# Kernel optimization log

Hardware: AMD Instinct MI355X
Metric: run time of the kernel (lower is better)

The kernel has to match this reference:

```python
import jax, jax.numpy as jnp
import numpy as np

B, N, D, R = 4, 50000, 64, 500
E_PER = 62500
E = B * E_PER


def _build_edges():
    rng = np.random.default_rng(0)
    idx = np.repeat(np.arange(B), E_PER)
    vi = rng.integers(0, N, E)
    vj = rng.integers(0, N, E)
    order = np.lexsort((vj, vi, idx))
    idx, vi, vj = idx[order], vi[order], vj[order]
    rel = rng.integers(0, R, E)
    key_vi = idx.astype(np.int64) * N + vi
    _, idx_vi = np.unique(key_vi, return_inverse=True)  # sorted -> nondecreasing segment ids
    key_vj = idx.astype(np.int64) * N + vj
    _, idx_vj = np.unique(key_vj, return_inverse=True)
    all_keys = np.concatenate([key_vi, key_vj])
    uniq_all, inv = np.unique(all_keys, return_inverse=True)
    e2vi, e2vj = inv[:E], inv[E:]
    sel = np.stack([idx, vi, vj, rel, idx_vi, idx_vj, e2vi, e2vj], axis=1).astype(np.int32)
    return sel, int(idx_vi.max() + 1), int(idx_vj.max() + 1), int(len(uniq_all))


def setup_inputs() -> dict:
    sel, n_vi_seg, n_vj_seg, n_visited = _build_edges()
    key = jax.random.key(0)
    ks = jax.random.split(key, 9)
    na = jax.random.uniform(ks[0], (B, N), jnp.float32) + 1e-6
    na = na / jnp.sum(na, axis=1, keepdims=True)
    return {
        'node_attention': na,
        'selected_edges': jnp.asarray(sel),
        'edges_y': jax.random.uniform(ks[1], (E,), jnp.float32, 0.1, 1.0),
        'hidden_con': jax.random.normal(ks[2], (n_visited, D), jnp.float32) * 0.1,
        'hidden_uncon': jax.random.normal(ks[3], (1, N, D), jnp.float32) * 0.1,
        'rel_emb': jax.random.normal(ks[4], (R, D), jnp.float32) * 0.1,
        'ws': jax.random.normal(ks[5], (8, D), jnp.float32) * (1.0 / np.sqrt(8.0)),
        'b': jax.random.normal(ks[6], (D,), jnp.float32) * 0.01,
        'out_w': jax.random.normal(ks[7], (D,), jnp.float32) * 0.3,
        'out_b': jax.random.normal(ks[8], (D,), jnp.float32) * 0.01,
        'n_vi_seg': n_vi_seg,
        'n_vj_seg': n_vj_seg,
    }


def reference(node_attention, selected_edges, edges_y, hidden_con, hidden_uncon,
              rel_emb, ws, b, out_w, out_b, n_vi_seg, n_vj_seg):
    idx, vi, vj = selected_edges[:, 0], selected_edges[:, 1], selected_edges[:, 2]
    rel, idx_vi, idx_vj = selected_edges[:, 3], selected_edges[:, 4], selected_edges[:, 5]
    e2vi, e2vj = selected_edges[:, 6], selected_edges[:, 7]

    # Node2Edge gathers
    hc_vi, hc_vj = hidden_con[e2vi], hidden_con[e2vj]        # [E, D]
    hu = hidden_uncon[0]                                     # hidden_uncon has batch 1
    hu_vi, hu_vj = hu[vi], hu[vj]                            # [E, D]
    re = rel_emb[rel]                                        # [E, D]

    # F layer: interact = [[0,3],[0,2,3],[0,4],[0,2,4],[1,3],[1,2,3],[1,4],[1,2,4]]
    terms = (hc_vi * hc_vj, hc_vi * re * hc_vj, hc_vi * hu_vj, hc_vi * re * hu_vj,
             hu_vi * hc_vj, hu_vi * re * hc_vj, hu_vi * hu_vj, hu_vi * re * hu_vj)
    f = b
    for k in range(8):
        f = f + ws[k] * terms[k]
    f = jax.nn.relu(f) * out_w + out_b                       # [E, D]
    logits = jnp.sum(f, axis=1)                              # [E]

    # NeighborSoftmax at='vi' (segment softmax)
    seg_max = jax.ops.segment_max(logits, idx_vi, num_segments=n_vi_seg)
    e = jnp.exp(logits - seg_max[idx_vi])
    es = jax.ops.segment_sum(e, idx_vi, num_segments=n_vi_seg)
    transition = e / es[idx_vi]

    # attention flow
    na_e = node_attention[idx, vi]
    ta = na_e * transition * edges_y

    # Aggregate at='vj', sum, then scatter into (B, n_nodes)
    aggr = jax.ops.segment_sum(ta, idx_vj, num_segments=n_vj_seg)
    seg_idx = jax.ops.segment_max(idx, idx_vj, num_segments=n_vj_seg)
    seg_vj = jax.ops.segment_max(vj, idx_vj, num_segments=n_vj_seg)
    Bn, Nn = node_attention.shape
    new_att = jnp.zeros((Bn, Nn), node_attention.dtype).at[seg_idx, seg_vj].add(aggr)
    return new_att / jnp.sum(new_att, axis=1, keepdims=True)
```

## Files before the change

### kernel.cpp

```cpp
#include <hip/hip_runtime.h>
#include <math.h>

#define D 64

__global__ __launch_bounds__(256) void k_logits(
    const int* __restrict__ sel, const float* __restrict__ hc,
    const float* __restrict__ hu, const float* __restrict__ re,
    const float* __restrict__ wsm, const float* __restrict__ bias,
    const float* __restrict__ out_w, const float* __restrict__ out_b,
    float* __restrict__ logits, int* __restrict__ seg_start,
    float* __restrict__ out, float* __restrict__ row_sum,
    int E, int BN, int Bn)
{
    const int tid = blockIdx.x * 256 + threadIdx.x;
    const int nthreads = gridDim.x * 256;

    for (int i = tid; i < BN; i += nthreads) out[i] = 0.f;
    if (tid < Bn) row_sum[tid] = 0.f;

    const int lane = threadIdx.x & 63;
    const int g    = lane >> 4;
    const int d16  = lane & 15;

    const float4* wsm4 = (const float4*)wsm;
    float4 W[8];
    #pragma unroll
    for (int k = 0; k < 8; ++k) W[k] = wsm4[k * 16 + d16];
    const float4 Bv = ((const float4*)bias)[d16];
    const float4 Ow = ((const float4*)out_w)[d16];
    const float4 Ob = ((const float4*)out_b)[d16];
    const float* Wf  = (const float*)W;
    const float* Bvf = (const float*)&Bv;
    const float* Owf = (const float*)&Ow;
    const float* Obf = (const float*)&Ob;

    const float4* hc4 = (const float4*)hc;
    const float4* hu4 = (const float4*)hu;
    const float4* re4 = (const float4*)re;

    const int wave   = tid >> 6;
    const int nwaves = nthreads >> 6;
    const int octs   = (E + 7) >> 3;

    for (int q = wave; q < octs; q += nwaves) {
        const int e0 = q * 8 + g;
        const int e1 = q * 8 + 4 + g;
        const bool v0 = (e0 < E);
        const bool v1 = (e1 < E);
        const int ec0 = v0 ? e0 : (E - 1);
        const int ec1 = v1 ? e1 : (E - 1);

        const int4 sA0 = *(const int4*)(sel + (size_t)ec0 * 8);
        const int4 sB0 = *(const int4*)(sel + (size_t)ec0 * 8 + 4);
        const int4 sA1 = *(const int4*)(sel + (size_t)ec1 * 8);
        const int4 sB1 = *(const int4*)(sel + (size_t)ec1 * 8 + 4);

        const float4 a0  = hc4[(size_t)sB0.z * 16 + d16];
        const float4 c0  = hc4[(size_t)sB0.w * 16 + d16];
        const float4 ui0 = hu4[(size_t)sA0.y * 16 + d16];
        const float4 uj0 = hu4[(size_t)sA0.z * 16 + d16];
        const float4 r0  = re4[(size_t)sA0.w * 16 + d16];
        const float4 a1  = hc4[(size_t)sB1.z * 16 + d16];
        const float4 c1  = hc4[(size_t)sB1.w * 16 + d16];
        const float4 ui1 = hu4[(size_t)sA1.y * 16 + d16];
        const float4 uj1 = hu4[(size_t)sA1.z * 16 + d16];
        const float4 r1  = re4[(size_t)sA1.w * 16 + d16];

        float acc0 = 0.f, acc1 = 0.f;
        {
            const float* ap = (const float*)&a0;  const float* cp = (const float*)&c0;
            const float* up = (const float*)&ui0; const float* vp = (const float*)&uj0;
            const float* rp = (const float*)&r0;
            #pragma unroll
            for (int k4 = 0; k4 < 4; ++k4) {
                const float hcvi = ap[k4], hcvj = cp[k4], huvi = up[k4], huvj = vp[k4], rr = rp[k4];
                const float hcr = hcvi * rr, hur = huvi * rr;
                float f = Bvf[k4];
                f += Wf[0*4+k4] * (hcvi * hcvj);
                f += Wf[1*4+k4] * (hcr  * hcvj);
                f += Wf[2*4+k4] * (hcvi * huvj);
                f += Wf[3*4+k4] * (hcr  * huvj);
                f += Wf[4*4+k4] * (huvi * hcvj);
                f += Wf[5*4+k4] * (hur  * hcvj);
                f += Wf[6*4+k4] * (huvi * huvj);
                f += Wf[7*4+k4] * (hur  * huvj);
                acc0 += fmaxf(f, 0.f) * Owf[k4] + Obf[k4];
            }
        }
        {
            const float* ap = (const float*)&a1;  const float* cp = (const float*)&c1;
            const float* up = (const float*)&ui1; const float* vp = (const float*)&uj1;
            const float* rp = (const float*)&r1;
            #pragma unroll
            for (int k4 = 0; k4 < 4; ++k4) {
                const float hcvi = ap[k4], hcvj = cp[k4], huvi = up[k4], huvj = vp[k4], rr = rp[k4];
                const float hcr = hcvi * rr, hur = huvi * rr;
                float f = Bvf[k4];
                f += Wf[0*4+k4] * (hcvi * hcvj);
                f += Wf[1*4+k4] * (hcr  * hcvj);
                f += Wf[2*4+k4] * (hcvi * huvj);
                f += Wf[3*4+k4] * (hcr  * huvj);
                f += Wf[4*4+k4] * (huvi * hcvj);
                f += Wf[5*4+k4] * (hur  * hcvj);
                f += Wf[6*4+k4] * (huvi * huvj);
                f += Wf[7*4+k4] * (hur  * huvj);
                acc1 += fmaxf(f, 0.f) * Owf[k4] + Obf[k4];
            }
        }

        #pragma unroll
        for (int off = 8; off > 0; off >>= 1) {
            acc0 += __shfl_xor(acc0, off, 64);
            acc1 += __shfl_xor(acc1, off, 64);
        }

        const int idxvi0 = sB0.x, idxvi1 = sB1.x;
        const int srcm16 = (lane >= 16) ? (lane - 16) : lane;
        const int p0w = __shfl(idxvi0, srcm16, 64);
        const int p1w = __shfl(idxvi1, srcm16, 64);
        const int p1b = __shfl(idxvi0, 48 + d16, 64);

        if (d16 == 0) {
            if (v0) {
                logits[e0] = acc0;
                int prev;
                if (e0 == 0)     prev = -1;
                else if (g == 0) prev = sel[(size_t)(e0 - 1) * 8 + 4];
                else             prev = p0w;
                if (idxvi0 != prev) seg_start[idxvi0] = e0;
                if (e0 == E - 1) seg_start[idxvi0 + 1] = E;
            }
            if (v1) {
                logits[e1] = acc1;
                const int prev = (g == 0) ? p1b : p1w;
                if (idxvi1 != prev) seg_start[idxvi1] = e1;
                if (e1 == E - 1) seg_start[idxvi1 + 1] = E;
            }
        }
    }
}

__global__ __launch_bounds__(256) void k_softmax_scatter(
    const int* __restrict__ sel, const float* __restrict__ logits,
    const int* __restrict__ seg_start, const float* __restrict__ na,
    const float* __restrict__ edges_y,
    float* __restrict__ out, int E, int N)
{
    const int e = blockIdx.x * 256 + threadIdx.x;
    if (e >= E) return;

    const int4 A = *(const int4*)(sel + (size_t)e * 8);
    const int  s = sel[(size_t)e * 8 + 4];
    const int start = seg_start[s];
    const int end   = seg_start[s + 1];

    const float myl  = logits[e];
    const float na_e = na[(size_t)A.x * N + A.y];
    const float ye   = edges_y[e];

    float m = myl;
    for (int i = start; i < end; ++i) m = fmaxf(m, logits[i]);
    float sum = 0.f;
    for (int i = start; i < end; ++i) sum += __expf(logits[i] - m);

    const float ta = na_e * (__expf(myl - m) / sum) * ye;
    atomicAdd(out + (size_t)A.x * N + A.z, ta);
}

__global__ __launch_bounds__(256) void k_rowsum(
    const float4* __restrict__ out, float* __restrict__ row_sum, int N4)
{
    __shared__ float red[4];
    const int row = blockIdx.y;
    float s = 0.f;
    for (int i = blockIdx.x * 256 + threadIdx.x; i < N4; i += gridDim.x * 256) {
        const float4 v = out[(size_t)row * N4 + i];
        s += v.x + v.y + v.z + v.w;
    }
    #pragma unroll
    for (int off = 32; off > 0; off >>= 1)
        s += __shfl_xor(s, off, 64);
    if ((threadIdx.x & 63) == 0) red[threadIdx.x >> 6] = s;
    __syncthreads();
    if (threadIdx.x == 0)
        atomicAdd(row_sum + row, red[0] + red[1] + red[2] + red[3]);
}

__global__ void k_norm(float4* __restrict__ out, const float* __restrict__ row_sum, int N4) {
    const int col = blockIdx.x * blockDim.x + threadIdx.x;
    const int row = blockIdx.y;
    if (col < N4) {
        const float inv = 1.f / row_sum[row];
        const size_t i = (size_t)row * N4 + col;
        float4 v = out[i];
        v.x *= inv; v.y *= inv; v.z *= inv; v.w *= inv;
        out[i] = v;
    }
}

extern "C" void kernel_launch(void* const* d_in, const int* in_sizes, int n_in,
                              void* d_out, int out_size, void* d_ws, size_t ws_size,
                              hipStream_t stream)
{
    const float* na    = (const float*)d_in[0];
    const int*   sel   = (const int*)  d_in[1];
    const float* ey    = (const float*)d_in[2];
    const float* hc    = (const float*)d_in[3];
    const float* hu    = (const float*)d_in[4];
    const float* re    = (const float*)d_in[5];
    const float* wsm   = (const float*)d_in[6];
    const float* bias  = (const float*)d_in[7];
    const float* ow    = (const float*)d_in[8];
    const float* ob    = (const float*)d_in[9];

    float* out = (float*)d_out;

    const int E  = in_sizes[2];
    const int N  = in_sizes[4] / D;
    const int BN = in_sizes[0];
    const int Bn = BN / N;

    float* logits    = (float*)d_ws;
    int*   seg_start = (int*)  ((char*)d_ws + (size_t)E * 4);
    const size_t rs_off = (((size_t)E * 8 + 4) + 255) & ~(size_t)255;
    float* row_sum   = (float*)((char*)d_ws + rs_off);

    k_logits<<<2048, 256, 0, stream>>>(sel, hc, hu, re, wsm, bias, ow, ob,
                                       logits, seg_start, out, row_sum, E, BN, Bn);
    k_softmax_scatter<<<(E + 255) / 256, 256, 0, stream>>>(sel, logits, seg_start, na, ey,
                                                           out, E, N);
    const int N4 = N / 4;
    dim3 rgrid(16, Bn);
    k_rowsum<<<rgrid, 256, 0, stream>>>((const float4*)out, row_sum, N4);
    dim3 ngrid((N4 + 255) / 256, Bn);
    k_norm<<<ngrid, 256, 0, stream>>>((float4*)out, row_sum, N4);
}
```

Baseline: 160.0 us.

## Prefetch next edge indices, factor relation term into weights, double logits grid

The logits kernel now loads the selected-edge index records for the next loop iteration before doing the current iteration's math. This is meant to hide the dependent index-then-gather latency chain. The eight-term feature sum is rewritten as four fused multiply-adds by folding the relation embedding into paired weights, which cuts ALU work per element. The launch grid is also doubled to raise the number of waves in flight. The prefetch costs extra registers, and with the larger grid each wave runs only a couple of iterations, so there is little left for the prefetch to overlap.

```diff
diff --git a/kernel.cpp b/kernel.cpp
--- a/kernel.cpp
+++ b/kernel.cpp
@@ -42,18 +42,21 @@
     const int nwaves = nthreads >> 6;
     const int octs   = (E + 7) >> 3;
 
-    for (int q = wave; q < octs; q += nwaves) {
+    int q = wave;
+    if (q >= octs) return;
+
+    int ec0 = min(q * 8 + g, E - 1);
+    int ec1 = min(q * 8 + 4 + g, E - 1);
+    int4 sA0 = *(const int4*)(sel + (size_t)ec0 * 8);
+    int4 sB0 = *(const int4*)(sel + (size_t)ec0 * 8 + 4);
+    int4 sA1 = *(const int4*)(sel + (size_t)ec1 * 8);
+    int4 sB1 = *(const int4*)(sel + (size_t)ec1 * 8 + 4);
+
+    for (; q < octs; q += nwaves) {
         const int e0 = q * 8 + g;
         const int e1 = q * 8 + 4 + g;
         const bool v0 = (e0 < E);
         const bool v1 = (e1 < E);
-        const int ec0 = v0 ? e0 : (E - 1);
-        const int ec1 = v1 ? e1 : (E - 1);
-
-        const int4 sA0 = *(const int4*)(sel + (size_t)ec0 * 8);
-        const int4 sB0 = *(const int4*)(sel + (size_t)ec0 * 8 + 4);
-        const int4 sA1 = *(const int4*)(sel + (size_t)ec1 * 8);
-        const int4 sB1 = *(const int4*)(sel + (size_t)ec1 * 8 + 4);
 
         const float4 a0  = hc4[(size_t)sB0.z * 16 + d16];
         const float4 c0  = hc4[(size_t)sB0.w * 16 + d16];
@@ -66,6 +69,19 @@
         const float4 uj1 = hu4[(size_t)sA1.z * 16 + d16];
         const float4 r1  = re4[(size_t)sA1.w * 16 + d16];
 
+        const int qn = q + nwaves;
+        int4 nA0, nB0, nA1, nB1;
+        const bool more = (qn < octs);
+        {
+            const int pe0 = more ? min(qn * 8 + g, E - 1) : ec0;
+            const int pe1 = more ? min(qn * 8 + 4 + g, E - 1) : ec1;
+            nA0 = *(const int4*)(sel + (size_t)pe0 * 8);
+            nB0 = *(const int4*)(sel + (size_t)pe0 * 8 + 4);
+            nA1 = *(const int4*)(sel + (size_t)pe1 * 8);
+            nB1 = *(const int4*)(sel + (size_t)pe1 * 8 + 4);
+            ec0 = pe0; ec1 = pe1;
+        }
+
         float acc0 = 0.f, acc1 = 0.f;
         {
             const float* ap = (const float*)&a0;  const float* cp = (const float*)&c0;
@@ -74,17 +90,16 @@
             #pragma unroll
             for (int k4 = 0; k4 < 4; ++k4) {
                 const float hcvi = ap[k4], hcvj = cp[k4], huvi = up[k4], huvj = vp[k4], rr = rp[k4];
-                const float hcr = hcvi * rr, hur = huvi * rr;
-                float f = Bvf[k4];
-                f += Wf[0*4+k4] * (hcvi * hcvj);
-                f += Wf[1*4+k4] * (hcr  * hcvj);
-                f += Wf[2*4+k4] * (hcvi * huvj);
-                f += Wf[3*4+k4] * (hcr  * huvj);
-                f += Wf[4*4+k4] * (huvi * hcvj);
-                f += Wf[5*4+k4] * (hur  * hcvj);
-                f += Wf[6*4+k4] * (huvi * huvj);
-                f += Wf[7*4+k4] * (hur  * huvj);
-                acc0 += fmaxf(f, 0.f) * Owf[k4] + Obf[k4];
+                const float p = hcvi * hcvj, qq = hcvi * huvj, ss = huvi * hcvj, uu = huvi * huvj;
+                const float w01 = fmaf(rr, Wf[1*4+k4], Wf[0*4+k4]);
+                const float w23 = fmaf(rr, Wf[3*4+k4], Wf[2*4+k4]);
+                const float w45 = fmaf(rr, Wf[5*4+k4], Wf[4*4+k4]);
+                const float w67 = fmaf(rr, Wf[7*4+k4], Wf[6*4+k4]);
+                float f = fmaf(p, w01, Bvf[k4]);
+                f = fmaf(qq, w23, f);
+                f = fmaf(ss, w45, f);
+                f = fmaf(uu, w67, f);
+                acc0 += fmaf(fmaxf(f, 0.f), Owf[k4], Obf[k4]);
             }
         }
         {
@@ -94,17 +109,16 @@
             #pragma unroll
             for (int k4 = 0; k4 < 4; ++k4) {
                 const float hcvi = ap[k4], hcvj = cp[k4], huvi = up[k4], huvj = vp[k4], rr = rp[k4];
-                const float hcr = hcvi * rr, hur = huvi * rr;
-                float f = Bvf[k4];
-                f += Wf[0*4+k4] * (hcvi * hcvj);
-                f += Wf[1*4+k4] * (hcr  * hcvj);
-                f += Wf[2*4+k4] * (hcvi * huvj);
-                f += Wf[3*4+k4] * (hcr  * huvj);
-                f += Wf[4*4+k4] * (huvi * hcvj);
-                f += Wf[5*4+k4] * (hur  * hcvj);
-                f += Wf[6*4+k4] * (huvi * huvj);
-                f += Wf[7*4+k4] * (hur  * huvj);
-                acc1 += fmaxf(f, 0.f) * Owf[k4] + Obf[k4];
+                const float p = hcvi * hcvj, qq = hcvi * huvj, ss = huvi * hcvj, uu = huvi * huvj;
+                const float w01 = fmaf(rr, Wf[1*4+k4], Wf[0*4+k4]);
+                const float w23 = fmaf(rr, Wf[3*4+k4], Wf[2*4+k4]);
+                const float w45 = fmaf(rr, Wf[5*4+k4], Wf[4*4+k4]);
+                const float w67 = fmaf(rr, Wf[7*4+k4], Wf[6*4+k4]);
+                float f = fmaf(p, w01, Bvf[k4]);
+                f = fmaf(qq, w23, f);
+                f = fmaf(ss, w45, f);
+                f = fmaf(uu, w67, f);
+                acc1 += fmaf(fmaxf(f, 0.f), Owf[k4], Obf[k4]);
             }
         }
 
@@ -137,6 +151,8 @@
                 if (e1 == E - 1) seg_start[idxvi1 + 1] = E;
             }
         }
+
+        sA0 = nA0; sB0 = nB0; sA1 = nA1; sB1 = nB1;
     }
 }
 
@@ -225,7 +241,7 @@
     const size_t rs_off = (((size_t)E * 8 + 4) + 255) & ~(size_t)255;
     float* row_sum   = (float*)((char*)d_ws + rs_off);
 
-    k_logits<<<2048, 256, 0, stream>>>(sel, hc, hu, re, wsm, bias, ow, ob,
+    k_logits<<<4096, 256, 0, stream>>>(sel, hc, hu, re, wsm, bias, ow, ob,
                                        logits, seg_start, out, row_sum, E, BN, Bn);
     k_softmax_scatter<<<(E + 255) / 256, 256, 0, stream>>>(sel, logits, seg_start, na, ey,
                                                            out, E, N);
```

Result: no change. 161.7 us (+1.1%).
